# Kernel tuning notes

Measured on AMD Instinct MI355X. Metric: run time of the kernel, lower is better.

Reference implementation:

```python
import jax, jax.numpy as jnp
import numpy as np

B, L = 4, 2048
D_Q = D_K = D_V = 512
D_MODEL = 512
H = 8  # heads; head dim = D_MODEL // H = 64


def _conv1x1(x, W, b):
    # Conv1d with kernel_size=1 == pointwise linear over channels.
    # x: (B, C_in, L), W: (C_out, C_in), b: (C_out,) -> (B, C_out, L)
    return jnp.einsum('oc,bcl->bol', W, x) + b[None, :, None]


def setup_inputs() -> dict:
    key = jax.random.key(0)
    ks = jax.random.split(key, 12)
    s = 0.02
    return {
        'q': jax.random.normal(ks[0], (B, D_Q, L), jnp.float32),
        'k': jax.random.normal(ks[1], (B, D_K, L), jnp.float32),
        'v': jax.random.normal(ks[2], (B, D_V, L), jnp.float32),
        'input_mask': jnp.ones((B, 1, L), jnp.float32),
        'Wq': jax.random.normal(ks[3], (D_MODEL, D_Q), jnp.float32) * s,
        'bq': jax.random.normal(ks[4], (D_MODEL,), jnp.float32) * s,
        'Wk': jax.random.normal(ks[5], (D_MODEL, D_K), jnp.float32) * s,
        'bk': jax.random.normal(ks[6], (D_MODEL,), jnp.float32) * s,
        'Wv': jax.random.normal(ks[7], (D_MODEL, D_V), jnp.float32) * s,
        'bv': jax.random.normal(ks[8], (D_MODEL,), jnp.float32) * s,
        'Wout': jax.random.normal(ks[9], (D_V, D_MODEL), jnp.float32) * s,
        'bout': jax.random.normal(ks[10], (D_V,), jnp.float32) * s,
    }


def reference(q, k, v, input_mask, Wq, bq, Wk, bk, Wv, bv, Wout, bout):
    Bq, _, Lq = q.shape
    qh = _conv1x1(q, Wq, bq).reshape(Bq, H, -1, Lq)  # (B,H,D,L)
    kh = _conv1x1(k, Wk, bk).reshape(Bq, H, -1, Lq)
    vh = _conv1x1(v, Wv, bv).reshape(Bq, H, -1, Lq)
    Dh = qh.shape[2]
    scale = 1.0 / jnp.sqrt(jnp.asarray(Dh, qh.dtype))
    scores = jnp.einsum('bhdl,bhdn->bhln', qh, kh) * scale  # (B,H,L,L)
    # total_mask = ~input_mask[:, 0:1, :].bool(); True -> masked keys
    pad = input_mask[:, 0:1, :] <= 0.5  # (B,1,L_k)
    scores = jnp.where(pad[:, None, :, :], jnp.asarray(-1e9, scores.dtype), scores)
    attn = jax.nn.softmax(scores, axis=-1)  # attn_dropout is None in module
    out = jnp.einsum('bhdn,bhln->bhdl', vh, attn).reshape(Bq, -1, Lq)  # (B,d_model,L)
    # self.dropout is identity at inference; final 1x1 conv projection
    return _conv1x1(out, Wout, bout)  # (B, d_v, L)
```

## Files before the change

### kernel.cpp

```cpp
#include <hip/hip_runtime.h>
#include <hip/hip_bf16.h>


#define BB  4
#define LL  2048
#define CC  512
#define HH  8
#define DHH 64

typedef __attribute__((ext_vector_type(8)))  short bf16x8;
typedef __attribute__((ext_vector_type(4)))  short bf16x4;
typedef __attribute__((ext_vector_type(16))) float f32x16;
typedef __attribute__((ext_vector_type(2)))  unsigned uint2v;
typedef __attribute__((ext_vector_type(4)))  unsigned uint4v;

using us = unsigned short;

#if __has_builtin(__builtin_amdgcn_exp2f)
#define EXP2(x) __builtin_amdgcn_exp2f(x)
#else
#define EXP2(x) __expf(0.6931471805599453f * (x))
#endif

__device__ __forceinline__ us f2bu(float x) {
    unsigned u = __float_as_uint(x);
    return (us)((u + 0x7FFFu + ((u >> 16) & 1u)) >> 16);
}
__device__ __forceinline__ unsigned pk2(float a, float b) {
    unsigned r;
    asm("v_cvt_pk_bf16_f32 %0, %1, %2" : "=v"(r) : "v"(a), "v"(b));
    return r;
}
__device__ __forceinline__ bf16x4 pk4(float a, float b, float c, float d) {
    uint2v u; u[0] = pk2(a, b); u[1] = pk2(c, d);
    return __builtin_bit_cast(bf16x4, u);
}

__device__ __forceinline__ void transpose_body(const float* __restrict__ X,
                                               us* __restrict__ Xt,
                                               int b, int c0, int n0, int t)
{
    __shared__ float T[64][65];

    const float* Xb = X + ((size_t)b * CC + c0) * LL + n0;
    #pragma unroll
    for (int i = 0; i < 4; ++i) {
        const int cl = (t >> 4) + 16 * i, nl = (t & 15) * 4;
        const float4 f = *(const float4*)(Xb + (size_t)cl * LL + nl);
        T[cl][nl + 0] = f.x; T[cl][nl + 1] = f.y;
        T[cl][nl + 2] = f.z; T[cl][nl + 3] = f.w;
    }
    __syncthreads();
    us* Ot = Xt + ((size_t)b * LL + n0) * CC + c0;
    #pragma unroll
    for (int i = 0; i < 2; ++i) {
        const int nl = (t >> 3) + 32 * i, cb = (t & 7) * 8;
        uint4v u;
        #pragma unroll
        for (int j = 0; j < 4; ++j)
            u[j] = pk2(T[cb + 2 * j][nl], T[cb + 2 * j + 1][nl]);
        *(bf16x8*)(Ot + (size_t)nl * CC + cb) = __builtin_bit_cast(bf16x8, u);
    }
}

__global__ __launch_bounds__(256) void transpose_cvt(const float* __restrict__ X,
                                                     us* __restrict__ Xt)
{
    transpose_body(X, Xt, blockIdx.z, blockIdx.y * 64, blockIdx.x * 64, threadIdx.x);
}

__global__ __launch_bounds__(256) void transpose_cvt3(
    const float* __restrict__ Xq, const float* __restrict__ Xk,
    const float* __restrict__ Xv,
    us* __restrict__ X0, us* __restrict__ X1, us* __restrict__ X2)
{
    const int z = blockIdx.z, which = z >> 2, b = z & 3;
    const float* X = which == 0 ? Xq : (which == 1 ? Xk : Xv);
    us* Xt = which == 0 ? X0 : (which == 1 ? X1 : X2);
    transpose_body(X, Xt, b, blockIdx.y * 64, blockIdx.x * 64, threadIdx.x);
}

__global__ __launch_bounds__(256) void cvt_w4(const float* __restrict__ W0,
                                              const float* __restrict__ W1,
                                              const float* __restrict__ W2,
                                              const float* __restrict__ W3,
                                              us* __restrict__ out)
{
    const float* Ws[4] = {W0, W1, W2, W3};
    const float* W = Ws[blockIdx.y];
    us* O = out + (size_t)blockIdx.y * (CC * CC);
    const int i = (blockIdx.x * 256 + threadIdx.x) * 8;
    const float4 f0 = *(const float4*)(W + i);
    const float4 f1 = *(const float4*)(W + i + 4);
    uint4v u;
    u[0] = pk2(f0.x, f0.y); u[1] = pk2(f0.z, f0.w);
    u[2] = pk2(f1.x, f1.y); u[3] = pk2(f1.z, f1.w);
    *(bf16x8*)(O + i) = __builtin_bit_cast(bf16x8, u);
}

__device__ __forceinline__ void proj_body(const us* __restrict__ Xb,
                                          const us* __restrict__ Wm,
                                          const float* __restrict__ bias,
                                          float scale, void* __restrict__ Yv,
                                          int b, int n0, int m0, int t, int mode)
{
    const int lane = t & 63, wave = t >> 6;
    const int quad2 = lane >> 5, l31 = lane & 31;
    const int wr = (wave >> 1) * 64, wc = (wave & 1) * 64;

    __shared__ __align__(16) char PS[66048];
    __shared__ float biasS[128];

    f32x16 acc[2][2];
    #pragma unroll
    for (int mi = 0; mi < 2; ++mi)
        #pragma unroll
        for (int ni = 0; ni < 2; ++ni)
            #pragma unroll
            for (int e = 0; e < 16; ++e) acc[mi][ni][e] = 0.f;

    if (t < 128) biasS[t] = bias[m0 + t];

    const int wrO = (t & 7) * 2064 + (t >> 3) * 16;
    const int rdA = quad2 * 2064 + (wr + l31) * 16;
    const int rdB = 16512 + quad2 * 2064 + (wc + l31) * 16;

    #pragma unroll
    for (int i = 0; i < 4; ++i) {
        const int r = i * 32 + (t >> 3), bk = t & 7;
        *(bf16x8*)(PS + wrO + i * 512) =
            *(const bf16x8*)(Wm + (size_t)r * CC + bk * 8);
        *(bf16x8*)(PS + 16512 + wrO + i * 512) =
            *(const bf16x8*)(Xb + (size_t)(n0 + r) * CC + bk * 8);
    }
    __syncthreads();

    for (int it = 0; it < CC / 64; ++it) {
        const int cur = it & 1, k1 = (it + 1) * 64;
        char* PB = PS + (cur ? 33024 : 0);
        char* PN = PS + (cur ? 0 : 33024);

        bf16x8 apre[4], bpre[4];
        if (it + 1 < CC / 64) {
            #pragma unroll
            for (int i = 0; i < 4; ++i) {
                const int r = i * 32 + (t >> 3), bk = t & 7;
                apre[i] = *(const bf16x8*)(Wm + (size_t)r * CC + k1 + bk * 8);
                bpre[i] = *(const bf16x8*)(Xb + (size_t)(n0 + r) * CC + k1 + bk * 8);
            }
        }

        __builtin_amdgcn_s_setprio(1);
        #pragma unroll
        for (int ks = 0; ks < 4; ++ks) {
            const bf16x8 af0 = *(const bf16x8*)(PB + rdA + ks * 4128);
            const bf16x8 af1 = *(const bf16x8*)(PB + rdA + ks * 4128 + 512);
            const bf16x8 bf0 = *(const bf16x8*)(PB + rdB + ks * 4128);
            const bf16x8 bf1 = *(const bf16x8*)(PB + rdB + ks * 4128 + 512);
            acc[0][0] = __builtin_amdgcn_mfma_f32_32x32x16_bf16(af0, bf0, acc[0][0], 0, 0, 0);
            acc[0][1] = __builtin_amdgcn_mfma_f32_32x32x16_bf16(af0, bf1, acc[0][1], 0, 0, 0);
            acc[1][0] = __builtin_amdgcn_mfma_f32_32x32x16_bf16(af1, bf0, acc[1][0], 0, 0, 0);
            acc[1][1] = __builtin_amdgcn_mfma_f32_32x32x16_bf16(af1, bf1, acc[1][1], 0, 0, 0);
        }
        __builtin_amdgcn_s_setprio(0);

        if (it + 1 < CC / 64) {
            #pragma unroll
            for (int i = 0; i < 4; ++i) {
                *(bf16x8*)(PN + wrO + i * 512) = apre[i];
                *(bf16x8*)(PN + 16512 + wrO + i * 512) = bpre[i];
            }
        }
        __syncthreads();
    }

    #pragma unroll
    for (int mi = 0; mi < 2; ++mi)
        #pragma unroll
        for (int ni = 0; ni < 2; ++ni) {
            const int nloc = wc + ni * 32 + l31;
            if (mode == 0) {
                us* Y = (us*)Yv;
                #pragma unroll
                for (int rg2 = 0; rg2 < 4; ++rg2) {
                    const int rbase = wr + mi * 32 + 8 * rg2 + 4 * quad2;
                    float v0 = (acc[mi][ni][rg2 * 4 + 0] + biasS[rbase + 0]) * scale;
                    float v1 = (acc[mi][ni][rg2 * 4 + 1] + biasS[rbase + 1]) * scale;
                    float v2 = (acc[mi][ni][rg2 * 4 + 2] + biasS[rbase + 2]) * scale;
                    float v3 = (acc[mi][ni][rg2 * 4 + 3] + biasS[rbase + 3]) * scale;
                    const int mg = m0 + rbase;
                    const int h = mg >> 6, d = mg & 63;
                    *(bf16x4*)(Y + (((size_t)(b * HH + h) * LL) + n0 + nloc) * DHH + d) =
                        pk4(v0, v1, v2, v3);
                }
            } else {
                #pragma unroll
                for (int reg = 0; reg < 16; ++reg) {
                    const int row = (reg & 3) + 8 * (reg >> 2) + 4 * quad2;
                    const int mloc = wr + mi * 32 + row;
                    const float v = (acc[mi][ni][reg] + biasS[mloc]) * scale;
                    const size_t addr = ((size_t)b * CC + m0 + mloc) * LL + n0 + nloc;
                    if (mode == 1) ((us*)Yv)[addr] = f2bu(v);
                    else           ((float*)Yv)[addr] = v;
                }
            }
        }
}

template <int MODE>
__global__ __launch_bounds__(256, 2) void proj_gemm(const us* __restrict__ Xt,
                                                    const us* __restrict__ Wb,
                                                    const float* __restrict__ bias,
                                                    float scale,
                                                    void* __restrict__ Yv)
{
    const int b = blockIdx.z, n0 = blockIdx.x * 128, m0 = blockIdx.y * 128;
    proj_body(Xt + (size_t)b * LL * CC, Wb + (size_t)m0 * CC, bias, scale, Yv,
              b, n0, m0, threadIdx.x, MODE);
}

__global__ __launch_bounds__(256, 2) void proj_gemm3(
    const us* __restrict__ X0, const us* __restrict__ X1, const us* __restrict__ X2,
    const us* __restrict__ Wb4,
    const float* __restrict__ bq, const float* __restrict__ bk,
    const float* __restrict__ bv, float scale_q,
    us* __restrict__ qh, us* __restrict__ kh, us* __restrict__ vh)
{
    const int z = blockIdx.z, which = z >> 2, b = z & 3;
    const int n0 = blockIdx.x * 128, m0 = blockIdx.y * 128;
    const us* Xt = which == 0 ? X0 : (which == 1 ? X1 : X2);
    const us* Wb = Wb4 + (size_t)which * (CC * CC);
    const float* bias = which == 0 ? bq : (which == 1 ? bk : bv);
    const float scale = which == 0 ? scale_q : 1.0f;
    us* Yv = which == 0 ? qh : (which == 1 ? kh : vh);
    const int mode = (which == 2) ? 1 : 0;
    proj_body(Xt + (size_t)b * LL * CC, Wb + (size_t)m0 * CC, bias, scale,
              (void*)Yv, b, n0, m0, threadIdx.x, mode);
}

__global__ __launch_bounds__(512, 4) void attn_fwd(
    const us* __restrict__ Qh,
    const us* __restrict__ Kh,
    const us* __restrict__ Vh,
    const float* __restrict__ mask,
    us* __restrict__ ctx)
{
    const int bh = blockIdx.x;
    const int b = bh >> 3, h = bh & 7;
    const int qb = blockIdx.y;
    const int t = threadIdx.x, lane = t & 63, wave = t >> 6;
    const int half = wave >> 2, wv = wave & 3;
    const int quad2 = lane >> 5, l31 = lane & 31;
    const int th = t & 255;

    __shared__ __align__(16) char SM[66560];
    unsigned long long* mwS = (unsigned long long*)(SM + 66304);

    const float* mb = mask + (size_t)b * LL;
    #pragma unroll
    for (int i = 0; i < 4; ++i) {
        const int tile = wave * 4 + i;
        const unsigned long long bal = __ballot(mb[tile * 64 + lane] > 0.5f);
        if (lane == 0) mwS[tile] = bal;
    }

    const us* Qg = Qh + ((size_t)bh * LL + qb * 128) * DHH;
    #pragma unroll
    for (int i = 0; i < 2; ++i) {
        const int c = t + i * 512, row = c & 127, bk = c >> 7;
        *(bf16x8*)(SM + c * 16) = *(const bf16x8*)(Qg + row * DHH + bk * 8);
    }

    const us* Kbase = Kh + (size_t)bh * LL * DHH;
    const us* Vbase = Vh + ((size_t)b * CC + h * DHH) * LL;
    char* KH = SM + 16384 + half * 16640;
    char* VH = SM + 49664 + half * 8320;
    const int wrO = (th & 7) * 1040 + (th >> 3) * 16;
    const int rdO = quad2 * 1040 + l31 * 16;
    const int qrd = quad2 * 2048 + (wv * 32 + l31) * 16;
    const int g0 = half * 16;

    #pragma unroll
    for (int i = 0; i < 2; ++i) {
        const int r = i * 32 + (th >> 3), bk = th & 7;
        *(bf16x8*)(KH + wrO + i * 512) =
            *(const bf16x8*)(Kbase + (size_t)(g0 * 64 + r) * DHH + bk * 8);
        *(bf16x8*)(VH + wrO + i * 512) =
            *(const bf16x8*)(Vbase + (size_t)r * LL + g0 * 64 + bk * 8);
    }
    __syncthreads();

    f32x16 of[2];
    #pragma unroll
    for (int mt = 0; mt < 2; ++mt)
        #pragma unroll
        for (int e = 0; e < 16; ++e) of[mt][e] = 0.f;
    float l_run = 0.f;

    for (int itl = 0; itl < 16; ++itl) {
        const int cur = itl & 1;
        char* Kc = KH + cur * 8320;
        char* Ka = KH + (1 - cur) * 8320;

        bf16x8 kpre[2], vpre[2];
        if (itl + 1 < 16) {
            const int n1 = (g0 + itl + 1) * 64;
            #pragma unroll
            for (int i = 0; i < 2; ++i) {
                const int r = i * 32 + (th >> 3), bk = th & 7;
                kpre[i] = *(const bf16x8*)(Kbase + (size_t)(n1 + r) * DHH + bk * 8);
                vpre[i] = *(const bf16x8*)(Vbase + (size_t)r * LL + n1 + bk * 8);
            }
        }

        f32x16 sf[2];
        #pragma unroll
        for (int mt = 0; mt < 2; ++mt)
            #pragma unroll
            for (int e = 0; e < 16; ++e) sf[mt][e] = 0.f;
        __builtin_amdgcn_s_setprio(1);
        #pragma unroll
        for (int ks = 0; ks < 4; ++ks) {
            const bf16x8 qk = *(const bf16x8*)(SM + qrd + ks * 4096);
            #pragma unroll
            for (int mt = 0; mt < 2; ++mt) {
                const bf16x8 af = *(const bf16x8*)(Kc + rdO + ks * 2080 + mt * 512);
                sf[mt] = __builtin_amdgcn_mfma_f32_32x32x16_bf16(af, qk, sf[mt], 0, 0, 0);
            }
        }
        __builtin_amdgcn_s_setprio(0);

        const unsigned long long mw = mwS[g0 + itl];
        const bool masked = (mw != 0xFFFFFFFFFFFFFFFFull);
        float ps = 0.f;
        bf16x8 pfrag[4];
        #pragma unroll
        for (int mt = 0; mt < 2; ++mt) {
            float p[16];
            #pragma unroll
            for (int e = 0; e < 16; ++e) p[e] = EXP2(sf[mt][e]);
            if (masked) {
                #pragma unroll
                for (int e = 0; e < 16; ++e) {
                    const int row = 32 * mt + (e & 3) + 8 * (e >> 2) + 4 * quad2;
                    p[e] = ((mw >> row) & 1ull) ? p[e] : 0.f;
                }
            }
            const float s0 = (p[0] + p[1]) + (p[2] + p[3]);
            const float s1 = (p[4] + p[5]) + (p[6] + p[7]);
            const float s2 = (p[8] + p[9]) + (p[10] + p[11]);
            const float s3 = (p[12] + p[13]) + (p[14] + p[15]);
            ps += (s0 + s1) + (s2 + s3);
            #pragma unroll
            for (int g = 0; g < 2; ++g) {
                unsigned w0 = pk2(p[8 * g + 0], p[8 * g + 1]);
                unsigned w1 = pk2(p[8 * g + 2], p[8 * g + 3]);
                unsigned w2 = pk2(p[8 * g + 4], p[8 * g + 5]);
                unsigned w3 = pk2(p[8 * g + 6], p[8 * g + 7]);
                asm("v_permlane32_swap_b32 %0, %1" : "+v"(w0), "+v"(w2));
                asm("v_permlane32_swap_b32 %0, %1" : "+v"(w1), "+v"(w3));
                uint4v u; u[0] = w0; u[1] = w1; u[2] = w2; u[3] = w3;
                pfrag[2 * mt + g] = __builtin_bit_cast(bf16x8, u);
            }
        }
        ps += __shfl_xor(ps, 32, 64);
        l_run += ps;

        __builtin_amdgcn_s_setprio(1);
        #pragma unroll
        for (int ks = 0; ks < 4; ++ks)
            #pragma unroll
            for (int mt = 0; mt < 2; ++mt) {
                const bf16x8 vf = *(const bf16x8*)(VH + rdO + ks * 2080 + mt * 512);
                of[mt] = __builtin_amdgcn_mfma_f32_32x32x16_bf16(vf, pfrag[ks], of[mt], 0, 0, 0);
            }
        __builtin_amdgcn_s_setprio(0);

        if (itl + 1 < 16) {
            #pragma unroll
            for (int i = 0; i < 2; ++i)
                *(bf16x8*)(Ka + wrO + i * 512) = kpre[i];
        }
        __syncthreads();
        if (itl + 1 < 16) {
            #pragma unroll
            for (int i = 0; i < 2; ++i)
                *(bf16x8*)(VH + wrO + i * 512) = vpre[i];
        }
        __syncthreads();
    }

    float4* OS = (float4*)SM;
    float*  LS = (float*)(SM + 32768);
    const int qg = qb * 128 + wv * 32;
    if (half == 1) {
        #pragma unroll
        for (int mt = 0; mt < 2; ++mt)
            #pragma unroll
            for (int r4 = 0; r4 < 4; ++r4) {
                float4 v;
                v.x = of[mt][r4 * 4 + 0]; v.y = of[mt][r4 * 4 + 1];
                v.z = of[mt][r4 * 4 + 2]; v.w = of[mt][r4 * 4 + 3];
                OS[(wv * 8 + mt * 4 + r4) * 64 + lane] = v;
            }
        LS[wv * 64 + lane] = l_run;
    }
    __syncthreads();
    if (half == 0) {
        l_run += LS[wv * 64 + lane];
        const float inv = 1.0f / l_run;
        us* Cb = ctx + (size_t)b * LL * CC;
        const int q = qg + l31;
        #pragma unroll
        for (int mt = 0; mt < 2; ++mt)
            #pragma unroll
            for (int r4 = 0; r4 < 4; ++r4) {
                const float4 v = OS[(wv * 8 + mt * 4 + r4) * 64 + lane];
                const int d = 32 * mt + 8 * r4 + 4 * quad2;
                *(bf16x4*)(Cb + (size_t)q * CC + h * DHH + d) =
                    pk4((of[mt][r4 * 4 + 0] + v.x) * inv,
                        (of[mt][r4 * 4 + 1] + v.y) * inv,
                        (of[mt][r4 * 4 + 2] + v.z) * inv,
                        (of[mt][r4 * 4 + 3] + v.w) * inv);
            }
    }
}

extern "C" void kernel_launch(void* const* d_in, const int* in_sizes, int n_in,
                              void* d_out, int out_size, void* d_ws, size_t ws_size,
                              hipStream_t stream)
{
    const float* q    = (const float*)d_in[0];
    const float* k    = (const float*)d_in[1];
    const float* v    = (const float*)d_in[2];
    const float* mask = (const float*)d_in[3];
    const float* Wq   = (const float*)d_in[4];
    const float* bq   = (const float*)d_in[5];
    const float* Wk   = (const float*)d_in[6];
    const float* bk   = (const float*)d_in[7];
    const float* Wv   = (const float*)d_in[8];
    const float* bv   = (const float*)d_in[9];
    const float* Wout = (const float*)d_in[10];
    const float* bout = (const float*)d_in[11];

    const size_t TSZ  = (size_t)BB * CC * LL;
    const size_t WSZ  = (size_t)4 * CC * CC;
    const float SCALE_Q = 0.125f * 1.4426950408889634f;

    const dim3 tb(256), gb(256);

    if (ws_size >= (6 * TSZ + WSZ) * sizeof(us)) {
        us* X0  = (us*)d_ws;
        us* X1  = X0 + TSZ;
        us* X2  = X1 + TSZ;
        us* qh  = X2 + TSZ;
        us* kh  = qh + TSZ;
        us* vh  = kh + TSZ;
        us* Wb  = vh + TSZ;
        us* ctx = X0;

        cvt_w4<<<dim3(CC * CC / 2048, 4), tb, 0, stream>>>(Wq, Wk, Wv, Wout, Wb);
        transpose_cvt3<<<dim3(LL / 64, CC / 64, 12), tb, 0, stream>>>(q, k, v, X0, X1, X2);
        proj_gemm3<<<dim3(LL / 128, CC / 128, 12), gb, 0, stream>>>(
            X0, X1, X2, Wb, bq, bk, bv, SCALE_Q, qh, kh, vh);
        attn_fwd<<<dim3(HH * BB, LL / 128), dim3(512), 0, stream>>>(qh, kh, vh, mask, ctx);
        proj_gemm<2><<<dim3(LL / 128, CC / 128, BB), gb, 0, stream>>>(
            ctx, Wb + 3 * (size_t)CC * CC, bout, 1.0f, d_out);
    } else {
        us* Xt  = (us*)d_ws;
        us* qh  = Xt + TSZ;
        us* kh  = qh + TSZ;
        us* vh  = kh + TSZ;
        us* Wb  = vh + TSZ;
        us* ctx = Xt;

        const dim3 tg(LL / 64, CC / 64, BB), gg(LL / 128, CC / 128, BB);

        cvt_w4<<<dim3(CC * CC / 2048, 4), tb, 0, stream>>>(Wq, Wk, Wv, Wout, Wb);
        transpose_cvt<<<tg, tb, 0, stream>>>(q, Xt);
        proj_gemm<0><<<gg, gb, 0, stream>>>(Xt, Wb + 0 * (size_t)CC * CC, bq, SCALE_Q, (void*)qh);
        transpose_cvt<<<tg, tb, 0, stream>>>(k, Xt);
        proj_gemm<0><<<gg, gb, 0, stream>>>(Xt, Wb + 1 * (size_t)CC * CC, bk, 1.0f, (void*)kh);
        transpose_cvt<<<tg, tb, 0, stream>>>(v, Xt);
        proj_gemm<1><<<gg, gb, 0, stream>>>(Xt, Wb + 2 * (size_t)CC * CC, bv, 1.0f, (void*)vh);
        attn_fwd<<<dim3(HH * BB, LL / 128), dim3(512), 0, stream>>>(qh, kh, vh, mask, ctx);
        proj_gemm<2><<<gg, gb, 0, stream>>>(ctx, Wb + 3 * (size_t)CC * CC, bout, 1.0f, d_out);
    }
}
```

Measured before the change: 192.9 us.

## Use direct global-to-LDS loads in projection and attention kernels

```diff
diff --git a/kernel.cpp b/kernel.cpp
--- a/kernel.cpp
+++ b/kernel.cpp
@@ -34,6 +34,12 @@
 __device__ __forceinline__ bf16x4 pk4(float a, float b, float c, float d) {
     uint2v u; u[0] = pk2(a, b); u[1] = pk2(c, d);
     return __builtin_bit_cast(bf16x4, u);
+}
+
+__device__ __forceinline__ void gl16(const void* g, void* l) {
+    __builtin_amdgcn_global_load_lds(
+        (const __attribute__((address_space(1))) unsigned int*)g,
+        (__attribute__((address_space(3))) unsigned int*)l, 16, 0, 0);
 }
 
 __device__ __forceinline__ void transpose_body(const float* __restrict__ X,
@@ -108,7 +114,7 @@
     const int quad2 = lane >> 5, l31 = lane & 31;
     const int wr = (wave >> 1) * 64, wc = (wave & 1) * 64;
 
-    __shared__ __align__(16) char PS[66048];
+    __shared__ __align__(16) char PS[32768];
     __shared__ float biasS[128];
 
     f32x16 acc[2][2];
@@ -121,56 +127,33 @@
 
     if (t < 128) biasS[t] = bias[m0 + t];
 
-    const int wrO = (t & 7) * 2064 + (t >> 3) * 16;
-    const int rdA = quad2 * 2064 + (wr + l31) * 16;
-    const int rdB = 16512 + quad2 * 2064 + (wc + l31) * 16;
-
-    #pragma unroll
-    for (int i = 0; i < 4; ++i) {
-        const int r = i * 32 + (t >> 3), bk = t & 7;
-        *(bf16x8*)(PS + wrO + i * 512) =
-            *(const bf16x8*)(Wm + (size_t)r * CC + bk * 8);
-        *(bf16x8*)(PS + 16512 + wrO + i * 512) =
-            *(const bf16x8*)(Xb + (size_t)(n0 + r) * CC + bk * 8);
-    }
-    __syncthreads();
-
-    for (int it = 0; it < CC / 64; ++it) {
-        const int cur = it & 1, k1 = (it + 1) * 64;
-        char* PB = PS + (cur ? 33024 : 0);
-        char* PN = PS + (cur ? 0 : 33024);
-
-        bf16x8 apre[4], bpre[4];
-        if (it + 1 < CC / 64) {
-            #pragma unroll
-            for (int i = 0; i < 4; ++i) {
-                const int r = i * 32 + (t >> 3), bk = t & 7;
-                apre[i] = *(const bf16x8*)(Wm + (size_t)r * CC + k1 + bk * 8);
-                bpre[i] = *(const bf16x8*)(Xb + (size_t)(n0 + r) * CC + k1 + bk * 8);
-            }
-        }
+    const int rdA = quad2 * 2048 + (wr + l31) * 16;
+    const int rdB = 16384 + quad2 * 2048 + (wc + l31) * 16;
+
+    for (int k0 = 0; k0 < CC; k0 += 64) {
+        #pragma unroll
+        for (int i = 0; i < 4; ++i) {
+            const int sg = i * 4 + wave;
+            const int r0 = (sg & 1) * 64, bk = sg >> 1;
+            gl16(Wm + (size_t)(r0 + lane) * CC + k0 + bk * 8, PS + sg * 1024);
+            gl16(Xb + (size_t)(n0 + r0 + lane) * CC + k0 + bk * 8,
+                 PS + 16384 + sg * 1024);
+        }
+        __syncthreads();
 
         __builtin_amdgcn_s_setprio(1);
         #pragma unroll
         for (int ks = 0; ks < 4; ++ks) {
-            const bf16x8 af0 = *(const bf16x8*)(PB + rdA + ks * 4128);
-            const bf16x8 af1 = *(const bf16x8*)(PB + rdA + ks * 4128 + 512);
-            const bf16x8 bf0 = *(const bf16x8*)(PB + rdB + ks * 4128);
-            const bf16x8 bf1 = *(const bf16x8*)(PB + rdB + ks * 4128 + 512);
+            const bf16x8 af0 = *(const bf16x8*)(PS + rdA + ks * 4096);
+            const bf16x8 af1 = *(const bf16x8*)(PS + rdA + ks * 4096 + 512);
+            const bf16x8 bf0 = *(const bf16x8*)(PS + rdB + ks * 4096);
+            const bf16x8 bf1 = *(const bf16x8*)(PS + rdB + ks * 4096 + 512);
             acc[0][0] = __builtin_amdgcn_mfma_f32_32x32x16_bf16(af0, bf0, acc[0][0], 0, 0, 0);
             acc[0][1] = __builtin_amdgcn_mfma_f32_32x32x16_bf16(af0, bf1, acc[0][1], 0, 0, 0);
             acc[1][0] = __builtin_amdgcn_mfma_f32_32x32x16_bf16(af1, bf0, acc[1][0], 0, 0, 0);
             acc[1][1] = __builtin_amdgcn_mfma_f32_32x32x16_bf16(af1, bf1, acc[1][1], 0, 0, 0);
         }
         __builtin_amdgcn_s_setprio(0);
-
-        if (it + 1 < CC / 64) {
-            #pragma unroll
-            for (int i = 0; i < 4; ++i) {
-                *(bf16x8*)(PN + wrO + i * 512) = apre[i];
-                *(bf16x8*)(PN + 16512 + wrO + i * 512) = bpre[i];
-            }
-        }
         __syncthreads();
     }
 
@@ -208,7 +191,7 @@
 }
 
 template <int MODE>
-__global__ __launch_bounds__(256, 2) void proj_gemm(const us* __restrict__ Xt,
+__global__ __launch_bounds__(256, 3) void proj_gemm(const us* __restrict__ Xt,
                                                     const us* __restrict__ Wb,
                                                     const float* __restrict__ bias,
                                                     float scale,
@@ -219,7 +202,7 @@
               b, n0, m0, threadIdx.x, MODE);
 }
 
-__global__ __launch_bounds__(256, 2) void proj_gemm3(
+__global__ __launch_bounds__(256, 3) void proj_gemm3(
     const us* __restrict__ X0, const us* __restrict__ X1, const us* __restrict__ X2,
     const us* __restrict__ Wb4,
     const float* __restrict__ bq, const float* __restrict__ bk,
@@ -251,18 +234,11 @@
     const int t = threadIdx.x, lane = t & 63, wave = t >> 6;
     const int half = wave >> 2, wv = wave & 3;
     const int quad2 = lane >> 5, l31 = lane & 31;
-    const int th = t & 255;
-
-    __shared__ __align__(16) char SM[66560];
-    unsigned long long* mwS = (unsigned long long*)(SM + 66304);
+
+    __shared__ __align__(16) char SM[81920];
 
     const float* mb = mask + (size_t)b * LL;
-    #pragma unroll
-    for (int i = 0; i < 4; ++i) {
-        const int tile = wave * 4 + i;
-        const unsigned long long bal = __ballot(mb[tile * 64 + lane] > 0.5f);
-        if (lane == 0) mwS[tile] = bal;
-    }
+    const int g0 = half * 16;
 
     const us* Qg = Qh + ((size_t)bh * LL + qb * 128) * DHH;
     #pragma unroll
@@ -273,21 +249,19 @@
 
     const us* Kbase = Kh + (size_t)bh * LL * DHH;
     const us* Vbase = Vh + ((size_t)b * CC + h * DHH) * LL;
-    char* KH = SM + 16384 + half * 16640;
-    char* VH = SM + 49664 + half * 8320;
-    const int wrO = (th & 7) * 1040 + (th >> 3) * 16;
-    const int rdO = quad2 * 1040 + l31 * 16;
-    const int qrd = quad2 * 2048 + (wv * 32 + l31) * 16;
-    const int g0 = half * 16;
-
-    #pragma unroll
-    for (int i = 0; i < 2; ++i) {
-        const int r = i * 32 + (th >> 3), bk = th & 7;
-        *(bf16x8*)(KH + wrO + i * 512) =
-            *(const bf16x8*)(Kbase + (size_t)(g0 * 64 + r) * DHH + bk * 8);
-        *(bf16x8*)(VH + wrO + i * 512) =
-            *(const bf16x8*)(Vbase + (size_t)r * LL + g0 * 64 + bk * 8);
-    }
+    char* KH = SM + 16384 + half * 16384;
+    char* VH = SM + 49152 + half * 16384;
+
+    {
+        const int n1 = g0 * 64;
+        #pragma unroll
+        for (int i = 0; i < 2; ++i) {
+            const int sg = i * 4 + wv;
+            gl16(Kbase + (size_t)(n1 + lane) * DHH + sg * 8, KH + sg * 1024);
+            gl16(Vbase + (size_t)lane * LL + n1 + sg * 8, VH + sg * 1024);
+        }
+    }
+    float mval = mb[g0 * 64 + lane];
     __syncthreads();
 
     f32x16 of[2];
@@ -297,20 +271,26 @@
         for (int e = 0; e < 16; ++e) of[mt][e] = 0.f;
     float l_run = 0.f;
 
+    const int rdKV = quad2 * 1024 + l31 * 16;
+    const int qrd  = quad2 * 2048 + (wv * 32 + l31) * 16;
+
     for (int itl = 0; itl < 16; ++itl) {
         const int cur = itl & 1;
-        char* Kc = KH + cur * 8320;
-        char* Ka = KH + (1 - cur) * 8320;
-
-        bf16x8 kpre[2], vpre[2];
+        const char* Kc = KH + cur * 8192;
+        const char* Vc = VH + cur * 8192;
+
+        float mnext = 0.f;
         if (itl + 1 < 16) {
             const int n1 = (g0 + itl + 1) * 64;
+            char* Kn = KH + (1 - cur) * 8192;
+            char* Vn = VH + (1 - cur) * 8192;
             #pragma unroll
             for (int i = 0; i < 2; ++i) {
-                const int r = i * 32 + (th >> 3), bk = th & 7;
-                kpre[i] = *(const bf16x8*)(Kbase + (size_t)(n1 + r) * DHH + bk * 8);
-                vpre[i] = *(const bf16x8*)(Vbase + (size_t)r * LL + n1 + bk * 8);
-            }
+                const int sg = i * 4 + wv;
+                gl16(Kbase + (size_t)(n1 + lane) * DHH + sg * 8, Kn + sg * 1024);
+                gl16(Vbase + (size_t)lane * LL + n1 + sg * 8, Vn + sg * 1024);
+            }
+            mnext = mb[(size_t)(g0 + itl + 1) * 64 + lane];
         }
 
         f32x16 sf[2];
@@ -324,69 +304,48 @@
             const bf16x8 qk = *(const bf16x8*)(SM + qrd + ks * 4096);
             #pragma unroll
             for (int mt = 0; mt < 2; ++mt) {
-                const bf16x8 af = *(const bf16x8*)(Kc + rdO + ks * 2080 + mt * 512);
+                const bf16x8 af = *(const bf16x8*)(Kc + rdKV + ks * 2048 + mt * 512);
                 sf[mt] = __builtin_amdgcn_mfma_f32_32x32x16_bf16(af, qk, sf[mt], 0, 0, 0);
             }
         }
         __builtin_amdgcn_s_setprio(0);
 
-        const unsigned long long mw = mwS[g0 + itl];
+        const unsigned long long mw = __ballot(mval > 0.5f);
         const bool masked = (mw != 0xFFFFFFFFFFFFFFFFull);
         float ps = 0.f;
-        bf16x8 pfrag[4];
-        #pragma unroll
-        for (int mt = 0; mt < 2; ++mt) {
-            float p[16];
-            #pragma unroll
-            for (int e = 0; e < 16; ++e) p[e] = EXP2(sf[mt][e]);
+        #pragma unroll
+        for (int j = 0; j < 4; ++j) {
+            const int mt = j >> 1, g = j & 1;
+            float p[8];
+            #pragma unroll
+            for (int el = 0; el < 8; ++el) p[el] = EXP2(sf[mt][8 * g + el]);
             if (masked) {
                 #pragma unroll
-                for (int e = 0; e < 16; ++e) {
-                    const int row = 32 * mt + (e & 3) + 8 * (e >> 2) + 4 * quad2;
-                    p[e] = ((mw >> row) & 1ull) ? p[e] : 0.f;
+                for (int el = 0; el < 8; ++el) {
+                    const int row = 32 * mt + 16 * g + (el & 3) + 8 * (el >> 2) + 4 * quad2;
+                    p[el] = ((mw >> row) & 1ull) ? p[el] : 0.f;
                 }
             }
-            const float s0 = (p[0] + p[1]) + (p[2] + p[3]);
-            const float s1 = (p[4] + p[5]) + (p[6] + p[7]);
-            const float s2 = (p[8] + p[9]) + (p[10] + p[11]);
-            const float s3 = (p[12] + p[13]) + (p[14] + p[15]);
-            ps += (s0 + s1) + (s2 + s3);
-            #pragma unroll
-            for (int g = 0; g < 2; ++g) {
-                unsigned w0 = pk2(p[8 * g + 0], p[8 * g + 1]);
-                unsigned w1 = pk2(p[8 * g + 2], p[8 * g + 3]);
-                unsigned w2 = pk2(p[8 * g + 4], p[8 * g + 5]);
-                unsigned w3 = pk2(p[8 * g + 6], p[8 * g + 7]);
-                asm("v_permlane32_swap_b32 %0, %1" : "+v"(w0), "+v"(w2));
-                asm("v_permlane32_swap_b32 %0, %1" : "+v"(w1), "+v"(w3));
-                uint4v u; u[0] = w0; u[1] = w1; u[2] = w2; u[3] = w3;
-                pfrag[2 * mt + g] = __builtin_bit_cast(bf16x8, u);
-            }
+            ps += ((p[0] + p[1]) + (p[2] + p[3])) + ((p[4] + p[5]) + (p[6] + p[7]));
+            unsigned w0 = pk2(p[0], p[1]);
+            unsigned w1 = pk2(p[2], p[3]);
+            unsigned w2 = pk2(p[4], p[5]);
+            unsigned w3 = pk2(p[6], p[7]);
+            asm("v_permlane32_swap_b32 %0, %1" : "+v"(w0), "+v"(w2));
+            asm("v_permlane32_swap_b32 %0, %1" : "+v"(w1), "+v"(w3));
+            uint4v u; u[0] = w0; u[1] = w1; u[2] = w2; u[3] = w3;
+            const bf16x8 pf = __builtin_bit_cast(bf16x8, u);
+            __builtin_amdgcn_s_setprio(1);
+            of[0] = __builtin_amdgcn_mfma_f32_32x32x16_bf16(
+                *(const bf16x8*)(Vc + rdKV + j * 2048), pf, of[0], 0, 0, 0);
+            of[1] = __builtin_amdgcn_mfma_f32_32x32x16_bf16(
+                *(const bf16x8*)(Vc + rdKV + j * 2048 + 512), pf, of[1], 0, 0, 0);
+            __builtin_amdgcn_s_setprio(0);
         }
         ps += __shfl_xor(ps, 32, 64);
         l_run += ps;
-
-        __builtin_amdgcn_s_setprio(1);
-        #pragma unroll
-        for (int ks = 0; ks < 4; ++ks)
-            #pragma unroll
-            for (int mt = 0; mt < 2; ++mt) {
-                const bf16x8 vf = *(const bf16x8*)(VH + rdO + ks * 2080 + mt * 512);
-                of[mt] = __builtin_amdgcn_mfma_f32_32x32x16_bf16(vf, pfrag[ks], of[mt], 0, 0, 0);
-            }
-        __builtin_amdgcn_s_setprio(0);
-
-        if (itl + 1 < 16) {
-            #pragma unroll
-            for (int i = 0; i < 2; ++i)
-                *(bf16x8*)(Ka + wrO + i * 512) = kpre[i];
-        }
-        __syncthreads();
-        if (itl + 1 < 16) {
-            #pragma unroll
-            for (int i = 0; i < 2; ++i)
-                *(bf16x8*)(VH + wrO + i * 512) = vpre[i];
-        }
+        mval = mnext;
+
         __syncthreads();
     }
 
```

After: 218.7 us. +13.4%, slower.
